# Kernel optimization log

Measured on AMD Instinct MI355X. Metric: run time of the kernel, lower is better.

## Reference

```python
import jax, jax.numpy as jnp
import numpy as np
from jax import lax

INF = 1e10
R = 20          # max_distance: EDT truncated at this radius (exact under clamp)
NUM_CLASSES = 19


def _pass1d(f, axis):
    """1D squared distance transform min_{|d|<=R} (d^2 + f[shifted]), truncated.
    f: [..., H, W] with 0 at 'source' pixels, INF elsewhere. Out-of-bounds = INF
    (matches scipy, which sees nothing beyond the array border)."""
    pad = [(0, 0)] * f.ndim
    pad[axis] = (R, R)
    fp = jnp.pad(f, pad, constant_values=INF)
    n = f.shape[axis]
    out = jnp.full_like(f, INF)
    for d in range(2 * R + 1):  # fixed small loop (41 iters), jit-unrolled
        shifted = lax.slice_in_dim(fp, d, d + n, axis=axis)
        out = jnp.minimum(out, shifted + float((d - R) ** 2))
    return out


def edt_trunc(mask):
    """Euclidean distance from each True pixel to nearest False pixel,
    truncated at R (False pixels get 0). mask: [..., H, W] bool."""
    f = jnp.where(mask, INF, 0.0).astype(jnp.float32)
    g = _pass1d(f, -2)
    g = _pass1d(g, -1)
    return jnp.sqrt(jnp.minimum(g, float(R * R)))


def compute_sdf(onehot_bool):
    """Signed distance: negdist - posdist, per [B,C,H,W] one-hot masks.
    Already truncated at +-R, matching clamp(-R, R) in the torch module."""
    posdist = edt_trunc(onehot_bool)    # distance inside FG to BG
    negdist = edt_trunc(~onehot_bool)   # distance inside BG to FG
    return negdist - posdist


def setup_inputs() -> dict:
    key = jax.random.key(0)
    k1, k2 = jax.random.split(key)
    logits = jax.random.normal(k1, (8, NUM_CLASSES, 256, 512), dtype=jnp.float32)
    targets = jax.random.randint(k2, (8, 256, 512), 0, NUM_CLASSES, dtype=jnp.int64)
    return {"logits": logits, "targets": targets}


def reference(logits, targets):
    C = logits.shape[1]
    probs = jax.nn.softmax(logits, axis=1)                       # [B,C,H,W]
    onehot = jax.nn.one_hot(targets, C, axis=1, dtype=jnp.bool_)  # [B,C,H,W]
    sdf = compute_sdf(onehot)
    sdf = jnp.clip(sdf, -float(R), float(R)) / float(R)
    # mean over spatial, sum over classes, mean over batch (reduction='mean')
    per_class = jnp.mean(probs * sdf, axis=(2, 3))               # [B,C]
    loss = jnp.sum(per_class, axis=1)                            # [B]
    return jnp.mean(loss)
```

## Files before the change

### kernel.cpp

```cpp
#include <hip/hip_runtime.h>
#include <hip/hip_bf16.h>
#include <math.h>

#define NCLS 19
#define BB   8
#define HH   256
#define WW   512
#define CAP2 400u
#define SEG  8
#define WPC  70

typedef unsigned short u16x2 __attribute__((ext_vector_type(2)));

static __device__ __forceinline__ unsigned umin32(unsigned a, unsigned b) { return a < b ? a : b; }
static __device__ __forceinline__ float fsqrt_fast(float x) { return __builtin_amdgcn_sqrtf(x); }

static __device__ __forceinline__ unsigned pk_add_s(unsigned v, unsigned c) {
    unsigned d; asm("v_pk_add_u16 %0, %1, %2" : "=v"(d) : "s"(c), "v"(v)); return d;
}
static __device__ __forceinline__ unsigned pk_minv(unsigned a, unsigned b) {
    unsigned d; asm("v_pk_min_u16 %0, %1, %2" : "=v"(d) : "v"(a), "v"(b)); return d;
}
static __device__ __forceinline__ unsigned pk_maxv(unsigned a, unsigned b) {
    unsigned d; asm("v_pk_max_u16 %0, %1, %2" : "=v"(d) : "v"(a), "v"(b)); return d;
}
static __device__ __forceinline__ unsigned pk_hmin(unsigned a) {
    unsigned d;
    asm("v_pk_min_u16 %0, %1, %1 op_sel:[1,0] op_sel_hi:[0,1]" : "=v"(d) : "v"(a));
    return d;
}
static __device__ __forceinline__ void sq8(unsigned x, unsigned& w0, unsigned& w1) {
    unsigned a = x & 0x00FF00FFu;
    unsigned b = (x >> 8) & 0x00FF00FFu;
    u16x2 sa = __builtin_bit_cast(u16x2, a); sa = sa * sa;
    u16x2 sb = __builtin_bit_cast(u16x2, b); sb = sb * sb;
    unsigned ua = __builtin_bit_cast(unsigned, sa);
    unsigned ub = __builtin_bit_cast(unsigned, sb);
    w0 = __builtin_amdgcn_perm(ub, ua, 0x05040100u);
    w1 = __builtin_amdgcn_perm(ub, ua, 0x07060302u);
}

__global__ __launch_bounds__(256)
void kA_vert(const int* __restrict__ targ, unsigned char* __restrict__ vneg,
             unsigned long long* __restrict__ acc) {
    if (blockIdx.x == 0 && threadIdx.x == 0) { *acc = 0ULL; }
    int gid = blockIdx.x * 256 + threadIdx.x;
    int col = gid & 4095;
    int seg = gid >> 12;
    int b = col >> 9;
    int w = col & 511;
    int h0 = seg * SEG;
    const int* tp = &targ[b * HH * WW + w];

    unsigned d[NCLS];
    unsigned pk[NCLS][2];
#pragma unroll
    for (int c = 0; c < NCLS; ++c) { d[c] = 21u; pk[c][0] = 0u; pk[c][1] = 0u; }
#pragma unroll
    for (int k = 0; k < 21 + SEG; ++k) {
        int hh = h0 - 21 + k;
        int t = -1;
        if (hh >= 0) t = tp[hh * WW];
#pragma unroll
        for (int c = 0; c < NCLS; ++c)
            d[c] = (t == c) ? 0u : d[c] + 1u;
        if (k >= 21) {
            int r = k - 21;
#pragma unroll
            for (int c = 0; c < NCLS; ++c)
                pk[c][r >> 2] |= d[c] << ((r & 3) * 8);
        }
    }
    unsigned u[NCLS];
#pragma unroll
    for (int c = 0; c < NCLS; ++c) u[c] = 21u;
#pragma unroll
    for (int k = 0; k < 21 + SEG; ++k) {
        int hh = h0 + 21 + SEG - 1 - k;
        int t = -1;
        if (hh < HH) t = tp[hh * WW];
#pragma unroll
        for (int c = 0; c < NCLS; ++c)
            u[c] = (t == c) ? 0u : u[c] + 1u;
        if (k >= 21) {
            int r = 21 + SEG - 1 - k;
#pragma unroll
            for (int c = 0; c < NCLS; ++c) {
                unsigned dv = (pk[c][r >> 2] >> ((r & 3) * 8)) & 0xffu;
                vneg[((size_t)(b * NCLS + c) * HH + hh) * WW + w] =
                    (unsigned char)umin32(dv, u[c]);
            }
        }
    }
}

__global__ __launch_bounds__(256)
void kB_main(const float* __restrict__ logits,
             const unsigned char* __restrict__ vneg,
             unsigned long long* __restrict__ acc) {
    __shared__ __align__(16) unsigned smem[NCLS * 280];
    int tid = threadIdx.x;
    int L = tid & 63;
    int wid = tid >> 6;
    int bh = blockIdx.x;
    int b = bh >> 8;
    int h = bh & 255;

    float (*sNum)[256] = (float (*)[256])smem;
    float (*sDen)[256] = (float (*)[256])(smem + 1024);
    float (*sEt)[256]  = (float (*)[256])(smem + 2048);
    unsigned short (*sM2)[256] = (unsigned short (*)[256])(smem + 3072);
    float* wsum = (float*)(smem + 3584);

#define SQx(x) ((unsigned)((x) * (x)))
#define PK2(a, bq) (SQx(a) | (SQx(bq) << 16))
    const unsigned CE[21] = {
        PK2(-20,-19), PK2(-18,-17), PK2(-16,-15), PK2(-14,-13), PK2(-12,-11),
        PK2(-10,-9),  PK2(-8,-7),   PK2(-6,-5),   PK2(-4,-3),   PK2(-2,-1),
        PK2(0,1),     PK2(2,3),     PK2(4,5),     PK2(6,7),     PK2(8,9),
        PK2(10,11),   PK2(12,13),   PK2(14,15),   PK2(16,17),   PK2(18,19),
        PK2(20,21) };
    const unsigned CO[21] = {
        PK2(-21,-20), PK2(-19,-18), PK2(-17,-16), PK2(-15,-14), PK2(-13,-12),
        PK2(-11,-10), PK2(-9,-8),   PK2(-7,-6),   PK2(-5,-4),   PK2(-3,-2),
        PK2(-1,0),    PK2(1,2),     PK2(3,4),     PK2(5,6),     PK2(7,8),
        PK2(9,10),    PK2(11,12),   PK2(13,14),   PK2(15,16),   PK2(17,18),
        PK2(19,20) };
#undef PK2
#undef SQx

    const unsigned HALO2 = 441u | (441u << 16);
    const float* lroww = &logits[((size_t)(b * NCLS + wid) * HH + h) * WW + 8 * L];
    int nc = (wid < 3) ? 5 : 4;

#pragma unroll 1
    for (int i = 0; i < nc; ++i) {
        int c = wid + 4 * i;
        uint2 v8 = ((const uint2*)vneg)[((size_t)(b * NCLS + c) * HH + h) * 64 + L];
        uint4 wq;
        sq8(v8.x, wq.x, wq.y);
        sq8(v8.y, wq.z, wq.w);
        ((uint4*)smem)[c * WPC + L + 3] = wq;
        if (L < 12) smem[c * 280 + L] = HALO2;
        if (L >= 52) smem[c * 280 + 216 + L] = HALO2;
    }

    float den[8], num[8], et[8];
    unsigned m2[8];
#pragma unroll
    for (int p = 0; p < 8; ++p) { den[p]=0.f; num[p]=0.f; et[p]=0.f; m2[p]=0xFFFFu; }

    float4 f0n = *(const float4*)lroww;
    float4 f1n = *(const float4*)(lroww + 4);

#pragma unroll 1
    for (int i = 0; i < nc; ++i) {
        int c = wid + 4 * i;
        float4 f0 = f0n, f1 = f1n;
        if (i + 1 < nc) {
            const float* ln = lroww + (size_t)(i + 1) * 4 * (HH * WW);
            f0n = *(const float4*)ln;
            f1n = *(const float4*)(ln + 4);
        }

        const uint4* basep = (const uint4*)smem + c * WPC + L;
        uint4 q0 = basep[0], q1 = basep[1], q2 = basep[2], q3 = basep[3],
              q4 = basep[4], q5 = basep[5], q6 = basep[6];
        unsigned W[28] = {q0.x,q0.y,q0.z,q0.w, q1.x,q1.y,q1.z,q1.w,
                          q2.x,q2.y,q2.z,q2.w, q3.x,q3.y,q3.z,q3.w,
                          q4.x,q4.y,q4.z,q4.w, q5.x,q5.y,q5.z,q5.w,
                          q6.x,q6.y,q6.z,q6.w};

        unsigned ae[4], ao[4];
#pragma unroll
        for (int r = 0; r < 4; ++r) { ae[r] = 0xFFFFFFFFu; ao[r] = 0xFFFFFFFFu; }

#pragma unroll
        for (int r = 0; r < 4; ++r)
#pragma unroll
            for (int m = 7; m <= 13; ++m) {
                ae[r] = pk_minv(ae[r], pk_add_s(W[r + m + 2], CE[m]));
                ao[r] = pk_minv(ao[r], pk_add_s(W[r + m + 2], CO[m]));
            }

        unsigned mx = pk_maxv(pk_maxv(pk_maxv(pk_hmin(ae[0]), pk_hmin(ao[0])),
                                      pk_maxv(pk_hmin(ae[1]), pk_hmin(ao[1]))),
                              pk_maxv(pk_maxv(pk_hmin(ae[2]), pk_hmin(ao[2])),
                                      pk_maxv(pk_hmin(ae[3]), pk_hmin(ao[3]))));
        if (!__all(mx <= (49u | (49u << 16)))) {
#pragma unroll
            for (int r = 0; r < 4; ++r) {
#pragma unroll
                for (int m = 0; m <= 6; ++m) {
                    ae[r] = pk_minv(ae[r], pk_add_s(W[r + m + 2], CE[m]));
                    ao[r] = pk_minv(ao[r], pk_add_s(W[r + m + 2], CO[m]));
                }
#pragma unroll
                for (int m = 14; m <= 20; ++m) {
                    ae[r] = pk_minv(ae[r], pk_add_s(W[r + m + 2], CE[m]));
                    ao[r] = pk_minv(ao[r], pk_add_s(W[r + m + 2], CO[m]));
                }
            }
        }

        float fx[8] = {f0.x, f0.y, f0.z, f0.w, f1.x, f1.y, f1.z, f1.w};
#pragma unroll
        for (int r = 0; r < 4; ++r) {
            unsigned nd0 = pk_hmin(ae[r]) & 0xFFFFu;
            unsigned nd1 = pk_hmin(ao[r]) & 0xFFFFu;
            float e0 = __expf(fx[2 * r]), e1 = __expf(fx[2 * r + 1]);
            den[2 * r] += e0; den[2 * r + 1] += e1;
            float s0 = fsqrt_fast((float)umin32(nd0, CAP2));
            float s1 = fsqrt_fast((float)umin32(nd1, CAP2));
            num[2 * r]     += e0 * s0;
            num[2 * r + 1] += e1 * s1;
            bool z0 = (nd0 == 0), z1 = (nd1 == 0);
            et[2 * r]     = z0 ? e0 : et[2 * r];
            et[2 * r + 1] = z1 ? e1 : et[2 * r + 1];
            m2[2 * r]     = umin32(m2[2 * r],     z0 ? 0xFFFFu : nd0);
            m2[2 * r + 1] = umin32(m2[2 * r + 1], z1 ? 0xFFFFu : nd1);
        }
    }

    __syncthreads();
    float vsum = 0.f;
#pragma unroll
    for (int pass = 0; pass < 2; ++pass) {
        if ((L >> 5) == pass) {
            int base = 8 * (L & 31);
            *(float4*)&sNum[wid][base]     = (float4){num[0], num[1], num[2], num[3]};
            *(float4*)&sNum[wid][base + 4] = (float4){num[4], num[5], num[6], num[7]};
            *(float4*)&sDen[wid][base]     = (float4){den[0], den[1], den[2], den[3]};
            *(float4*)&sDen[wid][base + 4] = (float4){den[4], den[5], den[6], den[7]};
            *(float4*)&sEt[wid][base]      = (float4){et[0], et[1], et[2], et[3]};
            *(float4*)&sEt[wid][base + 4]  = (float4){et[4], et[5], et[6], et[7]};
            uint4 mq;
            mq.x = m2[0] | (m2[1] << 16); mq.y = m2[2] | (m2[3] << 16);
            mq.z = m2[4] | (m2[5] << 16); mq.w = m2[6] | (m2[7] << 16);
            *(uint4*)&sM2[wid][base] = mq;
        }
        __syncthreads();
        {
            float N = sNum[0][tid] + sNum[1][tid] + sNum[2][tid] + sNum[3][tid];
            float D = sDen[0][tid] + sDen[1][tid] + sDen[2][tid] + sDen[3][tid];
            float E = sEt[0][tid] + sEt[1][tid] + sEt[2][tid] + sEt[3][tid];
            unsigned M = umin32(umin32((unsigned)sM2[0][tid], (unsigned)sM2[1][tid]),
                                umin32((unsigned)sM2[2][tid], (unsigned)sM2[3][tid]));
            vsum += (N - E * fsqrt_fast((float)umin32(M, CAP2))) / D;
        }
        __syncthreads();
    }

#pragma unroll
    for (int off = 32; off >= 1; off >>= 1) vsum += __shfl_down(vsum, off);
    if (L == 0) wsum[wid] = vsum;
    __syncthreads();
    if (tid == 0) {
        float s = (wsum[0] + wsum[1]) + (wsum[2] + wsum[3]);
        double q = (double)s * (68719476736.0 / 20.0);
        atomicAdd(acc, (unsigned long long)(long long)q);
    }
}

__global__ void kC_final(const unsigned long long* __restrict__ acc,
                         float* __restrict__ out) {
    long long iv = (long long)*acc;
    double v = (double)iv / 68719476736.0;
    out[0] = (float)(v / (double)((size_t)BB * HH * WW));
}

extern "C" void kernel_launch(void* const* d_in, const int* in_sizes, int n_in,
                              void* d_out, int out_size, void* d_ws, size_t ws_size,
                              hipStream_t stream) {
    const float* logits = (const float*)d_in[0];
    const int* targ = (const int*)d_in[1];
    unsigned char* wsb = (unsigned char*)d_ws;
    unsigned long long* acc = (unsigned long long*)wsb;
    unsigned char* vneg = wsb + 64;

    kA_vert<<<512, 256, 0, stream>>>(targ, vneg, acc);
    kB_main<<<BB * HH, 256, 0, stream>>>(logits, vneg, acc);
    kC_final<<<1, 1, 0, stream>>>(acc, (float*)d_out);
}
```

Baseline: 61.73 us.

## Batch vneg loads, defer halo LDS reads, and spread the atomic accumulator

The vneg row loads for all of a wave's classes are now issued together before squaring and storing to shared memory, so their global latencies overlap instead of being serialized per class. The outer shared-memory words of the window are read only when the wide-radius fallback path is taken, which cuts LDS traffic on the common path. The single global atomic accumulator is split into 64 slots indexed by block, and the final kernel sums them, to reduce atomic contention. This needs a larger workspace offset and a serial 64-element sum in the final kernel.

```diff
diff --git a/kernel.cpp b/kernel.cpp
--- a/kernel.cpp
+++ b/kernel.cpp
@@ -43,7 +43,7 @@
 __global__ __launch_bounds__(256)
 void kA_vert(const int* __restrict__ targ, unsigned char* __restrict__ vneg,
              unsigned long long* __restrict__ acc) {
-    if (blockIdx.x == 0 && threadIdx.x == 0) { *acc = 0ULL; }
+    if (blockIdx.x == 0 && threadIdx.x < 64) acc[threadIdx.x] = 0ULL;
     int gid = blockIdx.x * 256 + threadIdx.x;
     int col = gid & 4095;
     int seg = gid >> 12;
@@ -133,17 +133,23 @@
     const float* lroww = &logits[((size_t)(b * NCLS + wid) * HH + h) * WW + 8 * L];
     int nc = (wid < 3) ? 5 : 4;
 
-#pragma unroll 1
-    for (int i = 0; i < nc; ++i) {
-        int c = wid + 4 * i;
-        uint2 v8 = ((const uint2*)vneg)[((size_t)(b * NCLS + c) * HH + h) * 64 + L];
-        uint4 wq;
-        sq8(v8.x, wq.x, wq.y);
-        sq8(v8.y, wq.z, wq.w);
-        ((uint4*)smem)[c * WPC + L + 3] = wq;
-        if (L < 12) smem[c * 280 + L] = HALO2;
-        if (L >= 52) smem[c * 280 + 216 + L] = HALO2;
-    }
+    uint2 v8s[5];
+#pragma unroll
+    for (int i = 0; i < 5; ++i)
+        if (i < nc)
+            v8s[i] = ((const uint2*)vneg)
+                [((size_t)(b * NCLS + wid + 4 * i) * HH + h) * 64 + L];
+#pragma unroll
+    for (int i = 0; i < 5; ++i)
+        if (i < nc) {
+            int c = wid + 4 * i;
+            uint4 wq;
+            sq8(v8s[i].x, wq.x, wq.y);
+            sq8(v8s[i].y, wq.z, wq.w);
+            ((uint4*)smem)[c * WPC + L + 3] = wq;
+            if (L < 12) smem[c * 280 + L] = HALO2;
+            if (L >= 52) smem[c * 280 + 216 + L] = HALO2;
+        }
 
     float den[8], num[8], et[8];
     unsigned m2[8];
@@ -164,12 +170,11 @@
         }
 
         const uint4* basep = (const uint4*)smem + c * WPC + L;
-        uint4 q0 = basep[0], q1 = basep[1], q2 = basep[2], q3 = basep[3],
-              q4 = basep[4], q5 = basep[5], q6 = basep[6];
-        unsigned W[28] = {q0.x,q0.y,q0.z,q0.w, q1.x,q1.y,q1.z,q1.w,
-                          q2.x,q2.y,q2.z,q2.w, q3.x,q3.y,q3.z,q3.w,
-                          q4.x,q4.y,q4.z,q4.w, q5.x,q5.y,q5.z,q5.w,
-                          q6.x,q6.y,q6.z,q6.w};
+        uint4 q2 = basep[2], q3 = basep[3], q4 = basep[4];
+        unsigned W[28];
+        W[8]=q2.x;  W[9]=q2.y;  W[10]=q2.z; W[11]=q2.w;
+        W[12]=q3.x; W[13]=q3.y; W[14]=q3.z; W[15]=q3.w;
+        W[16]=q4.x; W[17]=q4.y; W[18]=q4.z; W[19]=q4.w;
 
         unsigned ae[4], ao[4];
 #pragma unroll
@@ -188,6 +193,11 @@
                               pk_maxv(pk_maxv(pk_hmin(ae[2]), pk_hmin(ao[2])),
                                       pk_maxv(pk_hmin(ae[3]), pk_hmin(ao[3]))));
         if (!__all(mx <= (49u | (49u << 16)))) {
+            uint4 q0 = basep[0], q1 = basep[1], q5 = basep[5], q6 = basep[6];
+            W[0]=q0.x;  W[1]=q0.y;  W[2]=q0.z;  W[3]=q0.w;
+            W[4]=q1.x;  W[5]=q1.y;  W[6]=q1.z;  W[7]=q1.w;
+            W[20]=q5.x; W[21]=q5.y; W[22]=q5.z; W[23]=q5.w;
+            W[24]=q6.x; W[25]=q6.y; W[26]=q6.z; W[27]=q6.w;
 #pragma unroll
             for (int r = 0; r < 4; ++r) {
 #pragma unroll
@@ -258,13 +268,14 @@
     if (tid == 0) {
         float s = (wsum[0] + wsum[1]) + (wsum[2] + wsum[3]);
         double q = (double)s * (68719476736.0 / 20.0);
-        atomicAdd(acc, (unsigned long long)(long long)q);
+        atomicAdd(&acc[bh & 63], (unsigned long long)(long long)q);
     }
 }
 
 __global__ void kC_final(const unsigned long long* __restrict__ acc,
                          float* __restrict__ out) {
-    long long iv = (long long)*acc;
+    long long iv = 0;
+    for (int i = 0; i < 64; ++i) iv += (long long)acc[i];
     double v = (double)iv / 68719476736.0;
     out[0] = (float)(v / (double)((size_t)BB * HH * WW));
 }
@@ -276,7 +287,7 @@
     const int* targ = (const int*)d_in[1];
     unsigned char* wsb = (unsigned char*)d_ws;
     unsigned long long* acc = (unsigned long long*)wsb;
-    unsigned char* vneg = wsb + 64;
+    unsigned char* vneg = wsb + 1024;
 
     kA_vert<<<512, 256, 0, stream>>>(targ, vneg, acc);
     kB_main<<<BB * HH, 256, 0, stream>>>(logits, vneg, acc);
```

Measured after the change: 57.50 us. 6.8% less time.
